# Kernel tuning notes

Hardware: AMD Instinct MI355X
Metric: run time of the kernel (lower is better)

The kernel has to match this reference:

```python
import jax, jax.numpy as jnp
import numpy as np

EPS_PEN = 1e-05


def _penalty(x):
    return jnp.sqrt(x + EPS_PEN)


def _warp(img, flow):
    """Bilinear warp (Resample2d): sample img at (x+u, y+v), clamped borders.
    img: (B,C,H,W), flow: (B,2,H,W) -> (B,C,H,W)."""
    B, C, H, W = img.shape
    xs = jnp.arange(W, dtype=flow.dtype)[None, None, :]  # (1,1,W)
    ys = jnp.arange(H, dtype=flow.dtype)[None, :, None]  # (1,H,1)
    x = xs + flow[:, 0]  # (B,H,W)
    y = ys + flow[:, 1]
    x0f = jnp.floor(x)
    y0f = jnp.floor(y)
    wx = x - x0f  # bilinear weights
    wy = y - y0f
    x0 = jnp.clip(x0f.astype(jnp.int32), 0, W - 1)
    x1 = jnp.clip(x0 + 1, 0, W - 1)
    y0 = jnp.clip(y0f.astype(jnp.int32), 0, H - 1)
    y1 = jnp.clip(y0 + 1, 0, H - 1)
    img_flat = img.reshape(B, C, H * W)

    def gather(yi, xi):
        idx = (yi * W + xi).reshape(B, 1, H * W)
        idx = jnp.broadcast_to(idx, (B, C, H * W))
        return jnp.take_along_axis(img_flat, idx, axis=2).reshape(B, C, H, W)

    v00 = gather(y0, x0)
    v01 = gather(y0, x1)
    v10 = gather(y1, x0)
    v11 = gather(y1, x1)
    wx = wx[:, None]  # (B,1,H,W)
    wy = wy[:, None]
    return ((1 - wy) * ((1 - wx) * v00 + wx * v01)
            + wy * ((1 - wx) * v10 + wx * v11))


def _energy(flow, img1, img2, alpha=1.0, beta=1.0):
    img2_warp = _warp(img2, flow)
    A = jnp.sum((img1 - img2_warp) ** 2, axis=1)          # (B,H,W)
    data_term = jnp.sum(_penalty(A), axis=(1, 2))          # (B,)
    # conv with kernel_dx == horizontal forward diff per channel; dy vertical
    dx = flow[:, :, :, 1:] - flow[:, :, :, :-1]            # (B,2,H,W-1)
    dy = flow[:, :, 1:, :] - flow[:, :, :-1, :]            # (B,2,H-1,W)
    Bx = jnp.pad(jnp.sum(dx ** 2, axis=1), ((0, 0), (0, 0), (0, 1)))
    By = jnp.pad(jnp.sum(dy ** 2, axis=1), ((0, 0), (0, 1), (0, 0)))
    smooth_term = jnp.sum(_penalty(Bx + By), axis=(1, 2))  # (B,)
    return alpha * data_term + beta * smooth_term


def setup_inputs() -> dict:
    key = jax.random.key(0)
    ks = jax.random.split(key, 6)
    B, H, W = 16, 448, 1024
    mean = jax.random.normal(ks[0], (B, 2, H, W), dtype=jnp.float32)
    log_var = jax.random.normal(ks[1], (B, 2, H, W), dtype=jnp.float32)
    img1 = jax.random.uniform(ks[2], (B, 3, H, W), dtype=jnp.float32)
    img2 = jax.random.uniform(ks[3], (B, 3, H, W), dtype=jnp.float32)
    target = jax.random.normal(ks[4], (B, 2, H, W), dtype=jnp.float32)
    eps = jax.random.normal(ks[5], (B, 2, H, W), dtype=jnp.float32)
    return {"mean": mean, "log_var": log_var, "img1": img1, "img2": img2,
            "target": target, "eps": eps}


def reference(mean, log_var, img1, img2, target, eps):
    # reparam: z = mean + exp(log_var/2) * eps  (eps replaces Normal(0,1).sample)
    flow_sample = mean + jnp.exp(log_var / 2.0) * eps
    elbo = _energy(flow_sample, img1, img2) - jnp.sum(log_var, axis=(1, 2, 3)) / 2.0
    mean_elbo = jnp.mean(elbo)
    # elementwise EPE: L2 norm over flow channels of (mean - target)
    epe = jnp.sqrt(jnp.sum((mean - target) ** 2, axis=1))
    mean_epe = jnp.mean(epe)
    return (mean_elbo, mean_epe)
```

## Files before the change

kernel.cpp:

```cpp
#include <hip/hip_runtime.h>

#define BB 16
#define HH 448
#define WW 1024
constexpr int HW    = HH * WW;
constexpr int ROWS  = 4;
constexpr int RGRP  = HH / ROWS;
constexpr int NBLK  = BB * RGRP;
constexpr int NTHR  = 256;
constexpr long long TOTAL = (long long)BB * HW;


__global__ __launch_bounds__(NTHR) void elbo_main(
    const float* __restrict__ mean, const float* __restrict__ lvar,
    const float* __restrict__ img1, const float* __restrict__ img2,
    const float* __restrict__ target, const float* __restrict__ eps,
    float2* __restrict__ partials)
{
    constexpr int NXCD = 8, CPX = NBLK / NXCD;
    const int wg = (blockIdx.x % NXCD) * CPX + blockIdx.x / NXCD;

    const int b  = wg / RGRP;
    const int y0 = (wg - b * RGRP) * ROWS;
    const int t  = threadIdx.x;
    const int x  = t << 2;

    const int fbase = b * 2 * HW;
    const int ibase = b * 3 * HW;

    float se = 0.f;
    float sp = 0.f;

    float u[4], v[4], un[4], vn[4];

    auto load_flow = [&](int y, float* uu, float* vv, bool contrib) {
        const int o = fbase + y * WW + x;
        const float4 m0 = *(const float4*)(mean + o);
        const float4 m1 = *(const float4*)(mean + o + HW);
        const float4 l0 = *(const float4*)(lvar + o);
        const float4 l1 = *(const float4*)(lvar + o + HW);
        const float4 e0 = *(const float4*)(eps  + o);
        const float4 e1 = *(const float4*)(eps  + o + HW);
        uu[0] = m0.x + __expf(0.5f * l0.x) * e0.x;
        uu[1] = m0.y + __expf(0.5f * l0.y) * e0.y;
        uu[2] = m0.z + __expf(0.5f * l0.z) * e0.z;
        uu[3] = m0.w + __expf(0.5f * l0.w) * e0.w;
        vv[0] = m1.x + __expf(0.5f * l1.x) * e1.x;
        vv[1] = m1.y + __expf(0.5f * l1.y) * e1.y;
        vv[2] = m1.z + __expf(0.5f * l1.z) * e1.z;
        vv[3] = m1.w + __expf(0.5f * l1.w) * e1.w;
        if (contrib) {
            const float4 t0 = *(const float4*)(target + o);
            const float4 t1 = *(const float4*)(target + o + HW);
            float du, dv;
            du = m0.x - t0.x; dv = m1.x - t1.x; sp += sqrtf(du*du + dv*dv);
            du = m0.y - t0.y; dv = m1.y - t1.y; sp += sqrtf(du*du + dv*dv);
            du = m0.z - t0.z; dv = m1.z - t1.z; sp += sqrtf(du*du + dv*dv);
            du = m0.w - t0.w; dv = m1.w - t1.w; sp += sqrtf(du*du + dv*dv);
            se -= 0.5f * (l0.x + l0.y + l0.z + l0.w +
                          l1.x + l1.y + l1.z + l1.w);
        }
    };

    load_flow(y0, u, v, true);

    for (int r = 0; r < ROWS; ++r) {
        const int y = y0 + r;
        const bool have_dn = (y + 1) < HH;
        if (have_dn) load_flow(y + 1, un, vn, r < ROWS - 1);

        float uR = __shfl_down(u[0], 1);
        float vR = __shfl_down(v[0], 1);
        if (((t & 63) == 63) && (t != NTHR - 1)) {
            const int o = fbase + y * WW + x + 4;
            uR = mean[o]      + __expf(0.5f * lvar[o])      * eps[o];
            vR = mean[o + HW] + __expf(0.5f * lvar[o + HW]) * eps[o + HW];
        }

        const int ro = y * WW + x;
        const float4 g0 = *(const float4*)(img1 + ibase + ro);
        const float4 g1 = *(const float4*)(img1 + ibase + HW + ro);
        const float4 g2 = *(const float4*)(img1 + ibase + 2 * HW + ro);
        const float i1c0[4] = {g0.x, g0.y, g0.z, g0.w};
        const float i1c1[4] = {g1.x, g1.y, g1.z, g1.w};
        const float i1c2[4] = {g2.x, g2.y, g2.z, g2.w};

        const float* __restrict__ p2 = img2 + ibase;

        #pragma unroll
        for (int i = 0; i < 4; ++i) {
            const float ui = u[i], vi = v[i];
            const int gx = x + i;

            float dx2 = 0.f, dy2 = 0.f;
            if (gx < WW - 1) {
                const float ur = (i < 3) ? u[i + 1] : uR;
                const float vr = (i < 3) ? v[i + 1] : vR;
                const float a = ur - ui, c = vr - vi;
                dx2 = a * a + c * c;
            }
            if (have_dn) {
                const float a = un[i] - ui, c = vn[i] - vi;
                dy2 = a * a + c * c;
            }
            se += sqrtf(dx2 + dy2 + 1e-5f);

            const float xs = (float)gx + ui;
            const float ys = (float)y  + vi;
            const float x0f = floorf(xs), y0f = floorf(ys);
            const float wx = xs - x0f,    wy = ys - y0f;
            int x0 = (int)x0f; x0 = min(max(x0, 0), WW - 1);
            const int x1 = min(x0 + 1, WW - 1);
            int yy0 = (int)y0f; yy0 = min(max(yy0, 0), HH - 1);
            const int yy1 = min(yy0 + 1, HH - 1);
            const int i00 = yy0 * WW + x0, i01 = yy0 * WW + x1;
            const int i10 = yy1 * WW + x0, i11 = yy1 * WW + x1;

            float A = 0.f;
            {
                const float v00 = p2[i00], v01 = p2[i01];
                const float v10 = p2[i10], v11 = p2[i11];
                const float top = v00 + wx * (v01 - v00);
                const float bot = v10 + wx * (v11 - v10);
                const float w   = top + wy * (bot - top);
                const float d   = i1c0[i] - w;
                A += d * d;
            }
            {
                const float v00 = p2[HW + i00], v01 = p2[HW + i01];
                const float v10 = p2[HW + i10], v11 = p2[HW + i11];
                const float top = v00 + wx * (v01 - v00);
                const float bot = v10 + wx * (v11 - v10);
                const float w   = top + wy * (bot - top);
                const float d   = i1c1[i] - w;
                A += d * d;
            }
            {
                const float v00 = p2[2*HW + i00], v01 = p2[2*HW + i01];
                const float v10 = p2[2*HW + i10], v11 = p2[2*HW + i11];
                const float top = v00 + wx * (v01 - v00);
                const float bot = v10 + wx * (v11 - v10);
                const float w   = top + wy * (bot - top);
                const float d   = i1c2[i] - w;
                A += d * d;
            }
            se += sqrtf(A + 1e-5f);
        }

        if (r < ROWS - 1) {
            #pragma unroll
            for (int i = 0; i < 4; ++i) { u[i] = un[i]; v[i] = vn[i]; }
        }
    }

    #pragma unroll
    for (int off = 32; off > 0; off >>= 1) {
        se += __shfl_down(se, off);
        sp += __shfl_down(sp, off);
    }
    __shared__ float s_e[NTHR / 64], s_p[NTHR / 64];
    const int lane = threadIdx.x & 63;
    const int wid  = threadIdx.x >> 6;
    if (lane == 0) { s_e[wid] = se; s_p[wid] = sp; }
    __syncthreads();
    if (threadIdx.x == 0) {
        float te = 0.0f, tp = 0.0f;
        #pragma unroll
        for (int i = 0; i < NTHR / 64; ++i) { te += s_e[i]; tp += s_p[i]; }
        partials[blockIdx.x] = make_float2(te, tp);
    }
}

__global__ __launch_bounds__(256) void elbo_final(
    const float2* __restrict__ partials, float* __restrict__ out)
{
    double se = 0.0, sp = 0.0;
    for (int i = threadIdx.x; i < NBLK; i += 256) {
        const float2 v = partials[i];
        se += (double)v.x;
        sp += (double)v.y;
    }
    #pragma unroll
    for (int off = 32; off > 0; off >>= 1) {
        se += __shfl_down(se, off);
        sp += __shfl_down(sp, off);
    }
    __shared__ double s_e[4], s_p[4];
    const int lane = threadIdx.x & 63;
    const int wid  = threadIdx.x >> 6;
    if (lane == 0) { s_e[wid] = se; s_p[wid] = sp; }
    __syncthreads();
    if (threadIdx.x == 0) {
        double te = 0.0, tp = 0.0;
        #pragma unroll
        for (int i = 0; i < 4; ++i) { te += s_e[i]; tp += s_p[i]; }
        out[0] = (float)(te / (double)BB);
        out[1] = (float)(tp / (double)TOTAL);
    }
}

extern "C" void kernel_launch(void* const* d_in, const int* in_sizes, int n_in,
                              void* d_out, int out_size, void* d_ws, size_t ws_size,
                              hipStream_t stream) {
    const float* mean   = (const float*)d_in[0];
    const float* logvar = (const float*)d_in[1];
    const float* img1   = (const float*)d_in[2];
    const float* img2   = (const float*)d_in[3];
    const float* target = (const float*)d_in[4];
    const float* eps    = (const float*)d_in[5];
    float* out = (float*)d_out;
    float2* partials = (float2*)d_ws;

    elbo_main<<<NBLK, NTHR, 0, stream>>>(mean, logvar, img1, img2, target, eps, partials);
    elbo_final<<<1, 256, 0, stream>>>(partials, out);
}
```

Baseline: 470.9 us.

## Process one image row per block instead of four rows

Each block now handles a single row rather than a strip of four rows, so the grid has four times as many blocks. The aim is more parallelism and latency hiding for the random img2 gathers, since the old per-block serial row loop chained loads. In exchange, the next-row flow (mean, log_var, eps) is recomputed in every block instead of being reused across the strip, which raises flow reads by up to 2x.

```diff
diff --git a/kernel.cpp b/kernel.cpp
--- a/kernel.cpp
+++ b/kernel.cpp
@@ -4,9 +4,7 @@
 #define HH 448
 #define WW 1024
 constexpr int HW    = HH * WW;
-constexpr int ROWS  = 4;
-constexpr int RGRP  = HH / ROWS;
-constexpr int NBLK  = BB * RGRP;
+constexpr int NBLK  = BB * HH;
 constexpr int NTHR  = 256;
 constexpr long long TOTAL = (long long)BB * HW;
 
@@ -20,137 +18,142 @@
     constexpr int NXCD = 8, CPX = NBLK / NXCD;
     const int wg = (blockIdx.x % NXCD) * CPX + blockIdx.x / NXCD;
 
-    const int b  = wg / RGRP;
-    const int y0 = (wg - b * RGRP) * ROWS;
-    const int t  = threadIdx.x;
-    const int x  = t << 2;
-
-    const int fbase = b * 2 * HW;
+    const int b = wg / HH;
+    const int y = wg - b * HH;
+    const int t = threadIdx.x;
+    const int x = t << 2;
+
+    const int o     = b * 2 * HW + y * WW + x;
     const int ibase = b * 3 * HW;
 
     float se = 0.f;
     float sp = 0.f;
 
-    float u[4], v[4], un[4], vn[4];
-
-    auto load_flow = [&](int y, float* uu, float* vv, bool contrib) {
-        const int o = fbase + y * WW + x;
-        const float4 m0 = *(const float4*)(mean + o);
-        const float4 m1 = *(const float4*)(mean + o + HW);
-        const float4 l0 = *(const float4*)(lvar + o);
-        const float4 l1 = *(const float4*)(lvar + o + HW);
-        const float4 e0 = *(const float4*)(eps  + o);
-        const float4 e1 = *(const float4*)(eps  + o + HW);
-        uu[0] = m0.x + __expf(0.5f * l0.x) * e0.x;
-        uu[1] = m0.y + __expf(0.5f * l0.y) * e0.y;
-        uu[2] = m0.z + __expf(0.5f * l0.z) * e0.z;
-        uu[3] = m0.w + __expf(0.5f * l0.w) * e0.w;
-        vv[0] = m1.x + __expf(0.5f * l1.x) * e1.x;
-        vv[1] = m1.y + __expf(0.5f * l1.y) * e1.y;
-        vv[2] = m1.z + __expf(0.5f * l1.z) * e1.z;
-        vv[3] = m1.w + __expf(0.5f * l1.w) * e1.w;
-        if (contrib) {
-            const float4 t0 = *(const float4*)(target + o);
-            const float4 t1 = *(const float4*)(target + o + HW);
-            float du, dv;
-            du = m0.x - t0.x; dv = m1.x - t1.x; sp += sqrtf(du*du + dv*dv);
-            du = m0.y - t0.y; dv = m1.y - t1.y; sp += sqrtf(du*du + dv*dv);
-            du = m0.z - t0.z; dv = m1.z - t1.z; sp += sqrtf(du*du + dv*dv);
-            du = m0.w - t0.w; dv = m1.w - t1.w; sp += sqrtf(du*du + dv*dv);
-            se -= 0.5f * (l0.x + l0.y + l0.z + l0.w +
-                          l1.x + l1.y + l1.z + l1.w);
-        }
-    };
-
-    load_flow(y0, u, v, true);
-
-    for (int r = 0; r < ROWS; ++r) {
-        const int y = y0 + r;
-        const bool have_dn = (y + 1) < HH;
-        if (have_dn) load_flow(y + 1, un, vn, r < ROWS - 1);
-
-        float uR = __shfl_down(u[0], 1);
-        float vR = __shfl_down(v[0], 1);
-        if (((t & 63) == 63) && (t != NTHR - 1)) {
-            const int o = fbase + y * WW + x + 4;
-            uR = mean[o]      + __expf(0.5f * lvar[o])      * eps[o];
-            vR = mean[o + HW] + __expf(0.5f * lvar[o + HW]) * eps[o + HW];
-        }
-
-        const int ro = y * WW + x;
-        const float4 g0 = *(const float4*)(img1 + ibase + ro);
-        const float4 g1 = *(const float4*)(img1 + ibase + HW + ro);
-        const float4 g2 = *(const float4*)(img1 + ibase + 2 * HW + ro);
-        const float i1c0[4] = {g0.x, g0.y, g0.z, g0.w};
-        const float i1c1[4] = {g1.x, g1.y, g1.z, g1.w};
-        const float i1c2[4] = {g2.x, g2.y, g2.z, g2.w};
-
-        const float* __restrict__ p2 = img2 + ibase;
-
-        #pragma unroll
-        for (int i = 0; i < 4; ++i) {
-            const float ui = u[i], vi = v[i];
-            const int gx = x + i;
-
-            float dx2 = 0.f, dy2 = 0.f;
-            if (gx < WW - 1) {
-                const float ur = (i < 3) ? u[i + 1] : uR;
-                const float vr = (i < 3) ? v[i + 1] : vR;
-                const float a = ur - ui, c = vr - vi;
-                dx2 = a * a + c * c;
-            }
-            if (have_dn) {
-                const float a = un[i] - ui, c = vn[i] - vi;
-                dy2 = a * a + c * c;
-            }
-            se += sqrtf(dx2 + dy2 + 1e-5f);
-
-            const float xs = (float)gx + ui;
-            const float ys = (float)y  + vi;
-            const float x0f = floorf(xs), y0f = floorf(ys);
-            const float wx = xs - x0f,    wy = ys - y0f;
-            int x0 = (int)x0f; x0 = min(max(x0, 0), WW - 1);
-            const int x1 = min(x0 + 1, WW - 1);
-            int yy0 = (int)y0f; yy0 = min(max(yy0, 0), HH - 1);
-            const int yy1 = min(yy0 + 1, HH - 1);
-            const int i00 = yy0 * WW + x0, i01 = yy0 * WW + x1;
-            const int i10 = yy1 * WW + x0, i11 = yy1 * WW + x1;
-
-            float A = 0.f;
-            {
-                const float v00 = p2[i00], v01 = p2[i01];
-                const float v10 = p2[i10], v11 = p2[i11];
-                const float top = v00 + wx * (v01 - v00);
-                const float bot = v10 + wx * (v11 - v10);
-                const float w   = top + wy * (bot - top);
-                const float d   = i1c0[i] - w;
-                A += d * d;
-            }
-            {
-                const float v00 = p2[HW + i00], v01 = p2[HW + i01];
-                const float v10 = p2[HW + i10], v11 = p2[HW + i11];
-                const float top = v00 + wx * (v01 - v00);
-                const float bot = v10 + wx * (v11 - v10);
-                const float w   = top + wy * (bot - top);
-                const float d   = i1c1[i] - w;
-                A += d * d;
-            }
-            {
-                const float v00 = p2[2*HW + i00], v01 = p2[2*HW + i01];
-                const float v10 = p2[2*HW + i10], v11 = p2[2*HW + i11];
-                const float top = v00 + wx * (v01 - v00);
-                const float bot = v10 + wx * (v11 - v10);
-                const float w   = top + wy * (bot - top);
-                const float d   = i1c2[i] - w;
-                A += d * d;
-            }
-            se += sqrtf(A + 1e-5f);
-        }
-
-        if (r < ROWS - 1) {
-            #pragma unroll
-            for (int i = 0; i < 4; ++i) { u[i] = un[i]; v[i] = vn[i]; }
-        }
+    const float4 m0 = *(const float4*)(mean + o);
+    const float4 m1 = *(const float4*)(mean + o + HW);
+    const float4 l0 = *(const float4*)(lvar + o);
+    const float4 l1 = *(const float4*)(lvar + o + HW);
+    const float4 e0 = *(const float4*)(eps  + o);
+    const float4 e1 = *(const float4*)(eps  + o + HW);
+
+    float u[4], v[4];
+    u[0] = m0.x + __expf(0.5f * l0.x) * e0.x;
+    u[1] = m0.y + __expf(0.5f * l0.y) * e0.y;
+    u[2] = m0.z + __expf(0.5f * l0.z) * e0.z;
+    u[3] = m0.w + __expf(0.5f * l0.w) * e0.w;
+    v[0] = m1.x + __expf(0.5f * l1.x) * e1.x;
+    v[1] = m1.y + __expf(0.5f * l1.y) * e1.y;
+    v[2] = m1.z + __expf(0.5f * l1.z) * e1.z;
+    v[3] = m1.w + __expf(0.5f * l1.w) * e1.w;
+
+    {
+        const float4 t0 = *(const float4*)(target + o);
+        const float4 t1 = *(const float4*)(target + o + HW);
+        float du, dv;
+        du = m0.x - t0.x; dv = m1.x - t1.x; sp += sqrtf(du*du + dv*dv);
+        du = m0.y - t0.y; dv = m1.y - t1.y; sp += sqrtf(du*du + dv*dv);
+        du = m0.z - t0.z; dv = m1.z - t1.z; sp += sqrtf(du*du + dv*dv);
+        du = m0.w - t0.w; dv = m1.w - t1.w; sp += sqrtf(du*du + dv*dv);
+        se -= 0.5f * (l0.x + l0.y + l0.z + l0.w +
+                      l1.x + l1.y + l1.z + l1.w);
+    }
+
+    const bool have_dn = (y + 1) < HH;
+    float un[4] = {0, 0, 0, 0}, vn[4] = {0, 0, 0, 0};
+    if (have_dn) {
+        const int od = o + WW;
+        const float4 dm0 = *(const float4*)(mean + od);
+        const float4 dm1 = *(const float4*)(mean + od + HW);
+        const float4 dl0 = *(const float4*)(lvar + od);
+        const float4 dl1 = *(const float4*)(lvar + od + HW);
+        const float4 de0 = *(const float4*)(eps  + od);
+        const float4 de1 = *(const float4*)(eps  + od + HW);
+        un[0] = dm0.x + __expf(0.5f * dl0.x) * de0.x;
+        un[1] = dm0.y + __expf(0.5f * dl0.y) * de0.y;
+        un[2] = dm0.z + __expf(0.5f * dl0.z) * de0.z;
+        un[3] = dm0.w + __expf(0.5f * dl0.w) * de0.w;
+        vn[0] = dm1.x + __expf(0.5f * dl1.x) * de1.x;
+        vn[1] = dm1.y + __expf(0.5f * dl1.y) * de1.y;
+        vn[2] = dm1.z + __expf(0.5f * dl1.z) * de1.z;
+        vn[3] = dm1.w + __expf(0.5f * dl1.w) * de1.w;
+    }
+
+    float uR = __shfl_down(u[0], 1);
+    float vR = __shfl_down(v[0], 1);
+    if (((t & 63) == 63) && (t != NTHR - 1)) {
+        const int o4 = o + 4;
+        uR = mean[o4]      + __expf(0.5f * lvar[o4])      * eps[o4];
+        vR = mean[o4 + HW] + __expf(0.5f * lvar[o4 + HW]) * eps[o4 + HW];
+    }
+
+    const int ro = y * WW + x;
+    const float4 g0 = *(const float4*)(img1 + ibase + ro);
+    const float4 g1 = *(const float4*)(img1 + ibase + HW + ro);
+    const float4 g2 = *(const float4*)(img1 + ibase + 2 * HW + ro);
+    const float i1c0[4] = {g0.x, g0.y, g0.z, g0.w};
+    const float i1c1[4] = {g1.x, g1.y, g1.z, g1.w};
+    const float i1c2[4] = {g2.x, g2.y, g2.z, g2.w};
+
+    const float* __restrict__ p2 = img2 + ibase;
+
+    #pragma unroll
+    for (int i = 0; i < 4; ++i) {
+        const float ui = u[i], vi = v[i];
+        const int gx = x + i;
+
+        float dx2 = 0.f, dy2 = 0.f;
+        if (gx < WW - 1) {
+            const float ur = (i < 3) ? u[i + 1] : uR;
+            const float vr = (i < 3) ? v[i + 1] : vR;
+            const float a = ur - ui, c = vr - vi;
+            dx2 = a * a + c * c;
+        }
+        if (have_dn) {
+            const float a = un[i] - ui, c = vn[i] - vi;
+            dy2 = a * a + c * c;
+        }
+        se += sqrtf(dx2 + dy2 + 1e-5f);
+
+        const float xs = (float)gx + ui;
+        const float ys = (float)y  + vi;
+        const float x0f = floorf(xs), y0f = floorf(ys);
+        const float wx = xs - x0f,    wy = ys - y0f;
+        int x0 = (int)x0f; x0 = min(max(x0, 0), WW - 1);
+        const int x1 = min(x0 + 1, WW - 1);
+        int yy0 = (int)y0f; yy0 = min(max(yy0, 0), HH - 1);
+        const int yy1 = min(yy0 + 1, HH - 1);
+        const int i00 = yy0 * WW + x0, i01 = yy0 * WW + x1;
+        const int i10 = yy1 * WW + x0, i11 = yy1 * WW + x1;
+
+        float A = 0.f;
+        {
+            const float v00 = p2[i00], v01 = p2[i01];
+            const float v10 = p2[i10], v11 = p2[i11];
+            const float top = v00 + wx * (v01 - v00);
+            const float bot = v10 + wx * (v11 - v10);
+            const float w   = top + wy * (bot - top);
+            const float d   = i1c0[i] - w;
+            A += d * d;
+        }
+        {
+            const float v00 = p2[HW + i00], v01 = p2[HW + i01];
+            const float v10 = p2[HW + i10], v11 = p2[HW + i11];
+            const float top = v00 + wx * (v01 - v00);
+            const float bot = v10 + wx * (v11 - v10);
+            const float w   = top + wy * (bot - top);
+            const float d   = i1c1[i] - w;
+            A += d * d;
+        }
+        {
+            const float v00 = p2[2*HW + i00], v01 = p2[2*HW + i01];
+            const float v10 = p2[2*HW + i10], v11 = p2[2*HW + i11];
+            const float top = v00 + wx * (v01 - v00);
+            const float bot = v10 + wx * (v11 - v10);
+            const float w   = top + wy * (bot - top);
+            const float d   = i1c2[i] - w;
+            A += d * d;
+        }
+        se += sqrtf(A + 1e-5f);
     }
 
     #pragma unroll
```

Result: no change. 477.5 us (+1.4%).
